# Kernel optimization log

Measured on AMD Instinct MI355X. Metric: run time of the kernel, lower is better.

The kernel has to match this reference:

```python
import jax, jax.numpy as jnp
import numpy as np

TRANSCRIBER_WEIGHT = 1.0
PREDICTOR_WEIGHT = 1.0


def setup_inputs() -> dict:
    key = jax.random.key(0)
    k1, k2, k3, k4 = jax.random.split(key, 4)
    B, T, U, D, V = 8, 256, 64, 512, 1024
    x = jax.random.normal(k1, (B, T, D), dtype=jnp.float32)   # transcriber output
    y = jax.random.normal(k2, (B, U, D), dtype=jnp.float32)   # predictor output
    # nn.Linear(D, V): weight [V, D], bias [V]
    W = jax.random.normal(k3, (V, D), dtype=jnp.float32) * (1.0 / np.sqrt(D))
    b = jax.random.normal(k4, (V,), dtype=jnp.float32) * 0.01
    return {"x": x, "y": y, "W": W, "b": b}


def reference(x, y, W, b):
    # h: [B, T, U, D] = tw * x[:, :, None, :] + pw * y[:, None, :, :]
    h = TRANSCRIBER_WEIGHT * x[:, :, None, :] + PREDICTOR_WEIGHT * y[:, None, :, :]
    h = jax.nn.relu(h)
    # linear: [B, T, U, V]
    return jnp.einsum('btud,vd->btuv', h, W) + b
```

## Files before the change

### kernel.cpp

```cpp
#include <hip/hip_runtime.h>
#include <hip/hip_bf16.h>


constexpr int Bc = 8, Tc = 256, Uc = 64, Dc = 512, Vc = 1024;
constexpr int BM = 64;
constexpr int NSTEPS = 16;
constexpr int BDIM = 1024;

typedef __attribute__((ext_vector_type(8)))  short short8;
typedef __attribute__((ext_vector_type(8)))  unsigned short ushort8;
typedef __attribute__((ext_vector_type(4)))  float f32x4;
typedef __attribute__((ext_vector_type(16))) float f32x16;
typedef __attribute__((ext_vector_type(4)))  unsigned int u32x4;

__device__ inline unsigned short f2bf(float f) {
    union { float f; unsigned u; } v; v.f = f;
    unsigned r = v.u + 0x7FFFu + ((v.u >> 16) & 1u);
    return (unsigned short)(r >> 16);
}

__device__ inline unsigned int pkbf(float lo, float hi) {
    unsigned int r;
    asm("v_cvt_pk_bf16_f32 %0, %1, %2" : "=v"(r) : "v"(lo), "v"(hi));
    return r;
}

__global__ __launch_bounds__(256) void cvt_wt(const float* __restrict__ W,
                                              unsigned short* __restrict__ Wt) {
    const int idx  = blockIdx.x * 256 + threadIdx.x;
    const int v    = idx >> 6;
    const int koct = idx & 63;
    const float4 a = *(const float4*)(W + (size_t)v * Dc + koct * 8);
    const float4 b = *(const float4*)(W + (size_t)v * Dc + koct * 8 + 4);
    ushort8 o;
    o[0] = f2bf(a.x); o[1] = f2bf(a.y); o[2] = f2bf(a.z); o[3] = f2bf(a.w);
    o[4] = f2bf(b.x); o[5] = f2bf(b.y); o[6] = f2bf(b.z); o[7] = f2bf(b.w);
    const size_t chunk = (size_t)(koct >> 1) * 2048 + v * 2 + (koct & 1);
    *(ushort8*)(Wt + chunk * 8) = o;
}

__global__ __launch_bounds__(BDIM, 4) void joiner_v14(
    const float* __restrict__ x, const float* __restrict__ y,
    const unsigned short* __restrict__ Wt, const float* __restrict__ bias,
    float* __restrict__ out)
{
    __shared__ __align__(16) unsigned char smem[BM * Dc * 2];
    unsigned short* As = (unsigned short*)smem;

    const int tid  = threadIdx.x;
    const int lane = tid & 63;
    const int wid  = tid >> 6;
    const int l31  = lane & 31;
    const int l32  = lane >> 5;

    const int mb = blockIdx.x;
    const int bb = mb >> 8;
    const int tt = mb & 255;
    const int m0 = mb * BM;
    const int colbase = wid * 64;

    float bv[2];
    bv[0] = bias[colbase + l31];
    bv[1] = bias[colbase + 32 + l31];

    const unsigned short* pW = Wt + (size_t)(colbase * 2 + 2 * l31 + l32) * 8;

    short8 wfA[2][2], wfB[2][2];

    #define LOADW(buf, ks)                                                    \
        {                                                                     \
            _Pragma("unroll")                                                 \
            for (int q = 0; q < 2; ++q)                                       \
                _Pragma("unroll")                                             \
                for (int n16 = 0; n16 < 2; ++n16)                             \
                    buf[q][n16] = *(const short8*)(pW + ((ks) * 2 + q) * 16384 \
                                                   + n16 * 512);              \
        }

    LOADW(wfA, 0);

    const float* xrow = x + (size_t)(bb * Tc + tt) * Dc;
    #pragma unroll
    for (int i = 0; i < 4; ++i) {
        const int c = tid + i * BDIM;
        const int u = c >> 6;
        const int s = c & 63;
        const float4* xp = (const float4*)(xrow + s * 8);
        const float4* yp = (const float4*)(y + ((size_t)(bb * Uc + u) * Dc + s * 8));
        float4 xa = xp[0], xb = xp[1];
        float4 ya = yp[0], yb = yp[1];
        u32x4 pv;
        pv[0] = pkbf(fmaxf(xa.x + ya.x, 0.f), fmaxf(xa.y + ya.y, 0.f));
        pv[1] = pkbf(fmaxf(xa.z + ya.z, 0.f), fmaxf(xa.w + ya.w, 0.f));
        pv[2] = pkbf(fmaxf(xb.x + yb.x, 0.f), fmaxf(xb.y + yb.y, 0.f));
        pv[3] = pkbf(fmaxf(xb.z + yb.z, 0.f), fmaxf(xb.w + yb.w, 0.f));
        *(u32x4*)(&As[u * Dc + ((s ^ (u & 7)) * 8)]) = pv;
    }
    __syncthreads();

    f32x16 acc[2][2] = {};

    #define STEP(cur, nxt, ks)                                                \
        {                                                                     \
            if ((ks) + 1 < NSTEPS) LOADW(nxt, (ks) + 1);                      \
            _Pragma("unroll")                                                 \
            for (int q = 0; q < 2; ++q) {                                     \
                const int oA = (ks) * 4 + q * 2 + l32;                        \
                short8 af0 = *(const short8*)(&As[l31 * Dc                    \
                                              + ((oA ^ (l31 & 7)) * 8)]);     \
                short8 af1 = *(const short8*)(&As[(32 + l31) * Dc             \
                                              + ((oA ^ (l31 & 7)) * 8)]);     \
                __builtin_amdgcn_s_setprio(1);                                \
                acc[0][0] = __builtin_amdgcn_mfma_f32_32x32x16_bf16(          \
                    af0, cur[q][0], acc[0][0], 0, 0, 0);                      \
                acc[0][1] = __builtin_amdgcn_mfma_f32_32x32x16_bf16(          \
                    af0, cur[q][1], acc[0][1], 0, 0, 0);                      \
                acc[1][0] = __builtin_amdgcn_mfma_f32_32x32x16_bf16(          \
                    af1, cur[q][0], acc[1][0], 0, 0, 0);                      \
                acc[1][1] = __builtin_amdgcn_mfma_f32_32x32x16_bf16(          \
                    af1, cur[q][1], acc[1][1], 0, 0, 0);                      \
                __builtin_amdgcn_s_setprio(0);                                \
            }                                                                 \
        }

    #pragma unroll
    for (int ks = 0; ks < NSTEPS; ks += 2) {
        STEP(wfA, wfB, ks);
        STEP(wfB, wfA, ks + 1);
    }
    #undef STEP
    #undef LOADW

    #pragma unroll
    for (int m16 = 0; m16 < 2; ++m16) {
        #pragma unroll
        for (int n16 = 0; n16 < 2; ++n16) {
            #pragma unroll
            for (int e = 0; e < 16; ++e) {
                const int rowl = (e & 3) + 8 * (e >> 2) + 4 * l32;
                const size_t off = (size_t)(m0 + m16 * 32 + rowl) * Vc
                                   + colbase + n16 * 32 + l31;
                __builtin_nontemporal_store(acc[m16][n16][e] + bv[n16], out + off);
            }
        }
    }
}

constexpr int F_BM = 128, F_BN = 128, F_BK = 64;
constexpr int F_MT = (Bc * Tc * Uc) / F_BM;
constexpr int F_NT = Vc / F_BN;

__global__ __launch_bounds__(256) void joiner_mfma(
    const float* __restrict__ x, const float* __restrict__ y,
    const float* __restrict__ W, const float* __restrict__ bias,
    float* __restrict__ out)
{
    __shared__ unsigned short As[F_BM * F_BK];
    __shared__ unsigned short Wsh[F_BN * F_BK];
    const int tid = threadIdx.x;
    const int mtile = blockIdx.x % F_MT;
    const int ntile = blockIdx.x / F_MT;
    const int m0 = mtile * F_BM, v0 = ntile * F_BN;
    const int bb = m0 / (Tc * Uc);
    const int t0 = (m0 % (Tc * Uc)) / Uc;
    const int lane = tid & 63, wid = tid >> 6;
    const int wm = wid >> 1, wn = wid & 1;
    const int lr = lane & 15, lk8 = lane >> 4;
    f32x4 acc[4][4] = {};
    for (int k0 = 0; k0 < Dc; k0 += F_BK) {
        __syncthreads();
        #pragma unroll
        for (int i = 0; i < 4; ++i) {
            const int chunk = tid + i * 256;
            const int row = chunk >> 3, slot = chunk & 7;
            const int ps8 = (slot ^ (row & 7)) * 8;
            const int t = t0 + (row >> 6), u = row & 63;
            const float4* xp = (const float4*)(x + ((size_t)(bb * Tc + t) * Dc + k0 + slot * 8));
            const float4* yp = (const float4*)(y + ((size_t)(bb * Uc + u) * Dc + k0 + slot * 8));
            float4 xa = xp[0], xb2 = xp[1], ya = yp[0], yb2 = yp[1];
            ushort8 hv;
            hv[0] = f2bf(fmaxf(xa.x + ya.x, 0.f)); hv[1] = f2bf(fmaxf(xa.y + ya.y, 0.f));
            hv[2] = f2bf(fmaxf(xa.z + ya.z, 0.f)); hv[3] = f2bf(fmaxf(xa.w + ya.w, 0.f));
            hv[4] = f2bf(fmaxf(xb2.x + yb2.x, 0.f)); hv[5] = f2bf(fmaxf(xb2.y + yb2.y, 0.f));
            hv[6] = f2bf(fmaxf(xb2.z + yb2.z, 0.f)); hv[7] = f2bf(fmaxf(xb2.w + yb2.w, 0.f));
            *(ushort8*)(&As[row * F_BK + ps8]) = hv;
            const float4* wp = (const float4*)(W + ((size_t)(v0 + row) * Dc + k0 + slot * 8));
            float4 wa = wp[0], wb2 = wp[1];
            ushort8 wv;
            wv[0] = f2bf(wa.x); wv[1] = f2bf(wa.y); wv[2] = f2bf(wa.z); wv[3] = f2bf(wa.w);
            wv[4] = f2bf(wb2.x); wv[5] = f2bf(wb2.y); wv[6] = f2bf(wb2.z); wv[7] = f2bf(wb2.w);
            *(ushort8*)(&Wsh[row * F_BK + ps8]) = wv;
        }
        __syncthreads();
        #pragma unroll
        for (int kk = 0; kk < 2; ++kk) {
            const int psk = kk * 4 + lk8;
            short8 af[4], bfr[4];
            #pragma unroll
            for (int mf = 0; mf < 4; ++mf) {
                const int row = wm * 64 + mf * 16 + lr;
                af[mf] = *(const short8*)(&As[row * F_BK + ((psk ^ (row & 7)) * 8)]);
            }
            #pragma unroll
            for (int nf = 0; nf < 4; ++nf) {
                const int row = wn * 64 + nf * 16 + lr;
                bfr[nf] = *(const short8*)(&Wsh[row * F_BK + ((psk ^ (row & 7)) * 8)]);
            }
            #pragma unroll
            for (int mf = 0; mf < 4; ++mf)
                #pragma unroll
                for (int nf = 0; nf < 4; ++nf)
                    acc[mf][nf] = __builtin_amdgcn_mfma_f32_16x16x32_bf16(af[mf], bfr[nf], acc[mf][nf], 0, 0, 0);
        }
    }
    #pragma unroll
    for (int nf = 0; nf < 4; ++nf) {
        const int v = v0 + wn * 64 + nf * 16 + lr;
        const float bv = bias[v];
        #pragma unroll
        for (int mf = 0; mf < 4; ++mf) {
            const int mrow = m0 + wm * 64 + mf * 16 + (lane >> 4) * 4;
            #pragma unroll
            for (int j = 0; j < 4; ++j)
                out[(size_t)(mrow + j) * Vc + v] = acc[mf][nf][j] + bv;
        }
    }
}

extern "C" void kernel_launch(void* const* d_in, const int* in_sizes, int n_in,
                              void* d_out, int out_size, void* d_ws, size_t ws_size,
                              hipStream_t stream) {
    const float* x = (const float*)d_in[0];
    const float* y = (const float*)d_in[1];
    const float* W = (const float*)d_in[2];
    const float* b = (const float*)d_in[3];
    float* out = (float*)d_out;

    const size_t w_bytes = (size_t)Vc * Dc * sizeof(unsigned short);
    if (ws_size >= w_bytes) {
        unsigned short* Wt = (unsigned short*)d_ws;
        cvt_wt<<<dim3((Vc * Dc / 8) / 256), 256, 0, stream>>>(W, Wt);
        joiner_v14<<<dim3(Bc * Tc * Uc / BM), BDIM, 0, stream>>>(x, y, Wt, b, out);
    } else {
        joiner_mfma<<<dim3(F_MT * F_NT), 256, 0, stream>>>(x, y, W, b, out);
    }
}
```

Measured before the change: 190.6 us.

## Split output columns across four blocks and stage the A tile in K halves

Each 1024-thread block is replaced by four 256-thread blocks, each computing a 256-column slice of V. The shared A tile is now staged in two K halves of 256, which cuts LDS per block from 64KB to 32KB so more blocks can be resident. In exchange, every block recomputes the relu(x+y) bf16 conversion for its 64 rows, giving four times the redundant staging work and x/y loads, and it adds extra barriers between the halves.

```diff
diff --git a/kernel.cpp b/kernel.cpp
--- a/kernel.cpp
+++ b/kernel.cpp
@@ -4,8 +4,8 @@
 
 constexpr int Bc = 8, Tc = 256, Uc = 64, Dc = 512, Vc = 1024;
 constexpr int BM = 64;
-constexpr int NSTEPS = 16;
-constexpr int BDIM = 1024;
+constexpr int KH = 256;
+constexpr int BDIM = 256;
 
 typedef __attribute__((ext_vector_type(8)))  short short8;
 typedef __attribute__((ext_vector_type(8)))  unsigned short ushort8;
@@ -39,13 +39,12 @@
     *(ushort8*)(Wt + chunk * 8) = o;
 }
 
-__global__ __launch_bounds__(BDIM, 4) void joiner_v14(
+__global__ __launch_bounds__(BDIM, 4) void joiner_v16(
     const float* __restrict__ x, const float* __restrict__ y,
     const unsigned short* __restrict__ Wt, const float* __restrict__ bias,
     float* __restrict__ out)
 {
-    __shared__ __align__(16) unsigned char smem[BM * Dc * 2];
-    unsigned short* As = (unsigned short*)smem;
+    __shared__ __align__(16) unsigned short As[BM * KH];
 
     const int tid  = threadIdx.x;
     const int lane = tid & 63;
@@ -53,11 +52,12 @@
     const int l31  = lane & 31;
     const int l32  = lane >> 5;
 
-    const int mb = blockIdx.x;
+    const int nq = blockIdx.x >> 11;
+    const int mb = blockIdx.x & 2047;
     const int bb = mb >> 8;
     const int tt = mb & 255;
     const int m0 = mb * BM;
-    const int colbase = wid * 64;
+    const int colbase = nq * 256 + wid * 64;
 
     float bv[2];
     bv[0] = bias[colbase + l31];
@@ -77,38 +77,38 @@
                                                    + n16 * 512);              \
         }
 
-    LOADW(wfA, 0);
-
     const float* xrow = x + (size_t)(bb * Tc + tt) * Dc;
-    #pragma unroll
-    for (int i = 0; i < 4; ++i) {
-        const int c = tid + i * BDIM;
-        const int u = c >> 6;
-        const int s = c & 63;
-        const float4* xp = (const float4*)(xrow + s * 8);
-        const float4* yp = (const float4*)(y + ((size_t)(bb * Uc + u) * Dc + s * 8));
-        float4 xa = xp[0], xb = xp[1];
-        float4 ya = yp[0], yb = yp[1];
-        u32x4 pv;
-        pv[0] = pkbf(fmaxf(xa.x + ya.x, 0.f), fmaxf(xa.y + ya.y, 0.f));
-        pv[1] = pkbf(fmaxf(xa.z + ya.z, 0.f), fmaxf(xa.w + ya.w, 0.f));
-        pv[2] = pkbf(fmaxf(xb.x + yb.x, 0.f), fmaxf(xb.y + yb.y, 0.f));
-        pv[3] = pkbf(fmaxf(xb.z + yb.z, 0.f), fmaxf(xb.w + yb.w, 0.f));
-        *(u32x4*)(&As[u * Dc + ((s ^ (u & 7)) * 8)]) = pv;
-    }
-    __syncthreads();
-
-    f32x16 acc[2][2] = {};
+    const float* yrow = y + (size_t)bb * Uc * Dc;
+    #define STAGE_HALF(h)                                                     \
+        {                                                                     \
+            _Pragma("unroll")                                                 \
+            for (int i = 0; i < 8; ++i) {                                     \
+                const int c = tid + i * BDIM;                                 \
+                const int u = c >> 5;                                         \
+                const int s = c & 31;                                         \
+                const float4* xp = (const float4*)(xrow + (h) * KH + s * 8);  \
+                const float4* yp = (const float4*)(yrow + (size_t)u * Dc      \
+                                                   + (h) * KH + s * 8);       \
+                float4 xa = xp[0], xb = xp[1];                                \
+                float4 ya = yp[0], yb = yp[1];                                \
+                u32x4 pv;                                                     \
+                pv[0] = pkbf(fmaxf(xa.x + ya.x, 0.f), fmaxf(xa.y + ya.y, 0.f)); \
+                pv[1] = pkbf(fmaxf(xa.z + ya.z, 0.f), fmaxf(xa.w + ya.w, 0.f)); \
+                pv[2] = pkbf(fmaxf(xb.x + yb.x, 0.f), fmaxf(xb.y + yb.y, 0.f)); \
+                pv[3] = pkbf(fmaxf(xb.z + yb.z, 0.f), fmaxf(xb.w + yb.w, 0.f)); \
+                *(u32x4*)(&As[u * KH + ((s ^ (u & 7)) * 8)]) = pv;            \
+            }                                                                 \
+        }
 
     #define STEP(cur, nxt, ks)                                                \
         {                                                                     \
-            if ((ks) + 1 < NSTEPS) LOADW(nxt, (ks) + 1);                      \
+            if ((ks) + 1 < 16) LOADW(nxt, (ks) + 1);                          \
             _Pragma("unroll")                                                 \
             for (int q = 0; q < 2; ++q) {                                     \
-                const int oA = (ks) * 4 + q * 2 + l32;                        \
-                short8 af0 = *(const short8*)(&As[l31 * Dc                    \
+                const int oA = ((ks) & 7) * 4 + q * 2 + l32;       \
+                short8 af0 = *(const short8*)(&As[l31 * KH                    \
                                               + ((oA ^ (l31 & 7)) * 8)]);     \
-                short8 af1 = *(const short8*)(&As[(32 + l31) * Dc             \
+                short8 af1 = *(const short8*)(&As[(32 + l31) * KH             \
                                               + ((oA ^ (l31 & 7)) * 8)]);     \
                 __builtin_amdgcn_s_setprio(1);                                \
                 acc[0][0] = __builtin_amdgcn_mfma_f32_32x32x16_bf16(          \
@@ -123,12 +123,27 @@
             }                                                                 \
         }
 
-    #pragma unroll
-    for (int ks = 0; ks < NSTEPS; ks += 2) {
+    LOADW(wfA, 0);
+    STAGE_HALF(0);
+    __syncthreads();
+
+    f32x16 acc[2][2] = {};
+
+    #pragma unroll
+    for (int ks = 0; ks < 8; ks += 2) {
         STEP(wfA, wfB, ks);
         STEP(wfB, wfA, ks + 1);
     }
+    __syncthreads();
+    STAGE_HALF(1);
+    __syncthreads();
+    #pragma unroll
+    for (int ks = 8; ks < 16; ks += 2) {
+        STEP(wfA, wfB, ks);
+        STEP(wfB, wfA, ks + 1);
+    }
     #undef STEP
+    #undef STAGE_HALF
     #undef LOADW
 
     #pragma unroll
@@ -240,7 +255,7 @@
     if (ws_size >= w_bytes) {
         unsigned short* Wt = (unsigned short*)d_ws;
         cvt_wt<<<dim3((Vc * Dc / 8) / 256), 256, 0, stream>>>(W, Wt);
-        joiner_v14<<<dim3(Bc * Tc * Uc / BM), BDIM, 0, stream>>>(x, y, Wt, b, out);
+        joiner_v16<<<dim3((Bc * Tc * Uc / BM) * 4), BDIM, 0, stream>>>(x, y, Wt, b, out);
     } else {
         joiner_mfma<<<dim3(F_MT * F_NT), 256, 0, stream>>>(x, y, W, b, out);
     }
```

After: 253.1 us. 1.33x slower.
